# Kernel optimization log

Measured on AMD Instinct MI355X. Metric: run time of the kernel, lower is better.

The kernel has to match this reference:

```python
import jax, jax.numpy as jnp
import numpy as np

TEMPERATURE = 0.07
EPS = 1e-07


def setup_inputs() -> dict:
    key = jax.random.key(0)
    kf, kl = jax.random.split(key)
    bsz, n_views, d = 4096, 2, 256
    feats = jax.random.normal(kf, (bsz, n_views, d), dtype=jnp.float32)
    # L2-normalize per view, as in standard SupCon pipelines
    feats = feats / jnp.linalg.norm(feats, axis=-1, keepdims=True)
    labels = jax.random.randint(kl, (bsz,), 0, 3, dtype=jnp.int64 if jax.config.jax_enable_x64 else jnp.int32)
    return {"features": feats, "labels": labels}


def reference(features, labels):
    bsz, n_views, d = features.shape
    n = bsz * n_views
    # torch.cat(torch.unbind(features, dim=1), dim=0): views stacked along batch
    contrast_feature = jnp.transpose(features, (1, 0, 2)).reshape(n, d)
    anchor_feature = contrast_feature  # contrast_mode == 'all'

    # label-equality mask with the module's 1e-7 offset, tiled over views
    mask_small = (labels[:, None] == labels[None, :]).astype(jnp.float32) + EPS
    mask = jnp.tile(mask_small, (n_views, n_views))  # [n, n]

    logits_mask = 1.0 - jnp.eye(n, dtype=jnp.float32)  # zero out self-contrast
    mask_pos = mask * logits_mask
    mask_neg = (1.0 - mask) * logits_mask

    similarity = jnp.exp(jnp.matmul(anchor_feature, contrast_feature.T) / TEMPERATURE)
    pos = jnp.sum(similarity * mask_pos, axis=1)
    neg = jnp.sum(similarity * mask_neg, axis=1)
    loss = -jnp.mean(jnp.log(pos / (pos + neg)))
    return loss
```

## Files before the change

### kernel.cpp

```cpp
#include <hip/hip_runtime.h>
#include <cstdint>

#define BSZ   4096
#define NTOT  8192
#define DIM   256
#define BT    128
#define BKE   64
#define NCB   (NTOT / BT)
#define INV_T (1.0f/0.07f)

typedef __bf16 bf16x8 __attribute__((ext_vector_type(8)));
typedef float  f32x4  __attribute__((ext_vector_type(4)));

#define GLOAD_LDS16(gp, lp)                                                  \
  __builtin_amdgcn_global_load_lds(                                          \
      (const __attribute__((address_space(1))) void*)(gp),                   \
      (__attribute__((address_space(3))) void*)(lp), 16, 0, 0)

__device__ __forceinline__ unsigned short f2bf(float f) {
  unsigned int u = __float_as_uint(f);
  u = u + 0x7FFFu + ((u >> 16) & 1u);
  return (unsigned short)(u >> 16);
}

__global__ __launch_bounds__(256) void cvt_kernel(const float* __restrict__ F,
                                                  unsigned short* __restrict__ X,
                                                  float* __restrict__ gsum,
                                                  int* __restrict__ gcnt) {
  if (blockIdx.x == 0 && threadIdx.x == 0) { *gsum = 0.f; *gcnt = 0; }
  int t = blockIdx.x * 256 + threadIdx.x;
  int r = t >> 6;
  int k = (t & 63) << 2;
  const float4 v = *(const float4*)(F + (size_t)(r & (BSZ - 1)) * (2 * DIM)
                                      + (r >> 12) * DIM + k);
  ushort4 o = make_ushort4(f2bf(v.x), f2bf(v.y), f2bf(v.z), f2bf(v.w));
  *(ushort4*)(X + (size_t)r * DIM + k) = o;
}

__global__ __launch_bounds__(256) void supcon_kernel(
    const unsigned short* __restrict__ X, const int* __restrict__ lab,
    float* __restrict__ partTot, float* __restrict__ partEq) {
  __shared__ unsigned short lA[BT * BKE];
  __shared__ unsigned short lB[BT * BKE];

  const int tid  = threadIdx.x;
  const int lane = tid & 63;
  const int wave = tid >> 6;
  const int wr   = (wave >> 1) * 64;
  const int wc   = (wave & 1) * 64;
  const int l15  = lane & 15;
  const int quad = lane >> 4;

  const int b = blockIdx.x;
  int j = (int)((sqrtf(8.f * (float)b + 1.f) - 1.f) * 0.5f);
  while ((j + 1) * (j + 2) / 2 <= b) ++j;
  while (j * (j + 1) / 2 > b) --j;
  const int i  = b - j * (j + 1) / 2;
  const int RB = i * BT;
  const int CB = j * BT;

  const int srow8  = lane >> 3;
  const int schunk = (lane & 7) ^ srow8;
  const unsigned short* gA = X + (size_t)(RB + wave * 32 + srow8) * DIM + schunk * 8;
  const unsigned short* gB = X + (size_t)(CB + wave * 32 + srow8) * DIM + schunk * 8;

  f32x4 acc[4][4] = {};

  for (int kb = 0; kb < DIM; kb += BKE) {
    __syncthreads();
#pragma unroll
    for (int l = 0; l < 4; ++l) {
      GLOAD_LDS16(gA + (size_t)l * 8 * DIM + kb, lA + (wave * 32 + l * 8) * BKE);
      GLOAD_LDS16(gB + (size_t)l * 8 * DIM + kb, lB + (wave * 32 + l * 8) * BKE);
    }
    __syncthreads();

#pragma unroll
    for (int sub = 0; sub < 2; ++sub) {
      bf16x8 aF[4], bF[4];
      const int slot = ((sub * 4 + quad) ^ (l15 & 7)) * 8;
#pragma unroll
      for (int t = 0; t < 4; ++t) {
        aF[t] = *(const bf16x8*)(lA + (wr + t * 16 + l15) * BKE + slot);
        bF[t] = *(const bf16x8*)(lB + (wc + t * 16 + l15) * BKE + slot);
      }
#pragma unroll
      for (int tr = 0; tr < 4; ++tr)
#pragma unroll
        for (int tc = 0; tc < 4; ++tc)
          acc[tr][tc] = __builtin_amdgcn_mfma_f32_16x16x32_bf16(
              aF[tr], bF[tc], acc[tr][tc], 0, 0, 0);
    }
  }

  int colIdx[4], colLab[4];
#pragma unroll
  for (int tc = 0; tc < 4; ++tc) {
    colIdx[tc] = CB + wc + tc * 16 + l15;
    colLab[tc] = lab[colIdx[tc] & (BSZ - 1)];
  }
  int rowLab[4][4];
#pragma unroll
  for (int tr = 0; tr < 4; ++tr)
#pragma unroll
    for (int reg = 0; reg < 4; ++reg)
      rowLab[tr][reg] = lab[(RB + wr + tr * 16 + quad * 4 + reg) & (BSZ - 1)];

  if (i == j) {
#pragma unroll
    for (int tr = 0; tr < 4; ++tr)
#pragma unroll
      for (int tc = 0; tc < 4; ++tc)
#pragma unroll
        for (int reg = 0; reg < 4; ++reg) {
          const int row = RB + wr + tr * 16 + quad * 4 + reg;
          float e = __expf(acc[tr][tc][reg] * INV_T);
          acc[tr][tc][reg] = (colIdx[tc] == row) ? 0.f : e;
        }
  } else {
#pragma unroll
    for (int tr = 0; tr < 4; ++tr)
#pragma unroll
      for (int tc = 0; tc < 4; ++tc)
#pragma unroll
        for (int reg = 0; reg < 4; ++reg)
          acc[tr][tc][reg] = __expf(acc[tr][tc][reg] * INV_T);
  }

  __syncthreads();
  float* sbuf = (float*)lA;
#pragma unroll
  for (int tr = 0; tr < 4; ++tr) {
#pragma unroll
    for (int reg = 0; reg < 4; ++reg) {
      float tot = 0.f, eqs = 0.f;
#pragma unroll
      for (int tc = 0; tc < 4; ++tc) {
        const float e = acc[tr][tc][reg];
        tot += e;
        if (colLab[tc] == rowLab[tr][reg]) eqs += e;
      }
#pragma unroll
      for (int off = 1; off < 16; off <<= 1) {
        tot += __shfl_xor(tot, off, 64);
        eqs += __shfl_xor(eqs, off, 64);
      }
      if (l15 == 0) {
        const int rl_ = wr + tr * 16 + quad * 4 + reg;
        sbuf[(wave & 1) * 128 + rl_]       = tot;
        sbuf[256 + (wave & 1) * 128 + rl_] = eqs;
      }
    }
  }
  if (i != j) {
#pragma unroll
    for (int tc = 0; tc < 4; ++tc) {
      float tt = 0.f, te = 0.f;
#pragma unroll
      for (int tr = 0; tr < 4; ++tr)
#pragma unroll
        for (int reg = 0; reg < 4; ++reg) {
          const float e = acc[tr][tc][reg];
          tt += e;
          if (rowLab[tr][reg] == colLab[tc]) te += e;
        }
      tt += __shfl_xor(tt, 16, 64);  te += __shfl_xor(te, 16, 64);
      tt += __shfl_xor(tt, 32, 64);  te += __shfl_xor(te, 32, 64);
      if (quad == 0) {
        const int cl_ = wc + tc * 16 + l15;
        sbuf[512 + (wave >> 1) * 128 + cl_] = tt;
        sbuf[768 + (wave >> 1) * 128 + cl_] = te;
      }
    }
  }
  __syncthreads();

  if (tid < 128) {
    partTot[(size_t)j * NTOT + RB + tid] = sbuf[tid] + sbuf[128 + tid];
    partEq [(size_t)j * NTOT + RB + tid] = sbuf[256 + tid] + sbuf[384 + tid];
  } else if (i != j) {
    const int c = tid - 128;
    partTot[(size_t)i * NTOT + CB + c] = sbuf[512 + c] + sbuf[640 + c];
    partEq [(size_t)i * NTOT + CB + c] = sbuf[768 + c] + sbuf[896 + c];
  }
}

__global__ __launch_bounds__(256) void reduce_kernel(
    const float* __restrict__ partTot, const float* __restrict__ partEq,
    float* __restrict__ gsum, int* __restrict__ gcnt,
    unsigned int* __restrict__ out) {
  const int r = blockIdx.x * 256 + threadIdx.x;
  float tot = 0.f, eqs = 0.f;
#pragma unroll 8
  for (int cb = 0; cb < NCB; ++cb) {
    tot += partTot[(size_t)cb * NTOT + r];
    eqs += partEq [(size_t)cb * NTOT + r];
  }
  const float term = __logf((eqs + 1e-7f * tot) / tot);
  __shared__ float red[256];
  red[threadIdx.x] = term;
  __syncthreads();
  for (int step = 128; step > 0; step >>= 1) {
    if (threadIdx.x < step) red[threadIdx.x] += red[threadIdx.x + step];
    __syncthreads();
  }
  if (threadIdx.x == 0) {
    atomicAdd(gsum, red[0]);
    __threadfence();
    const int old = atomicAdd(gcnt, 1);
    if (old == (int)gridDim.x - 1) {
      __threadfence();
      const float total = atomicAdd(gsum, 0.0f);
      const float loss = -total / (float)NTOT;
      const unsigned short bb = f2bf(loss);
      out[0] = ((unsigned int)bb << 16) | (unsigned int)bb;
    }
  }
}

extern "C" void kernel_launch(void* const* d_in, const int* in_sizes, int n_in,
                              void* d_out, int out_size, void* d_ws, size_t ws_size,
                              hipStream_t stream) {
  (void)in_sizes; (void)n_in; (void)out_size; (void)ws_size;
  const float* feats = (const float*)d_in[0];
  const int*   labels = (const int*)d_in[1];

  char* ws = (char*)d_ws;
  unsigned short* X = (unsigned short*)ws;
  float* partTot = (float*)(ws + (size_t)NTOT * DIM * 2);
  float* partEq  = partTot + (size_t)NCB * NTOT;
  float* gsum    = partEq  + (size_t)NCB * NTOT;
  int*   gcnt    = (int*)(gsum + 1);

  cvt_kernel<<<NTOT * DIM / 4 / 256, 256, 0, stream>>>(feats, X, gsum, gcnt);
  supcon_kernel<<<NCB * (NCB + 1) / 2, 256, 0, stream>>>(X, labels, partTot, partEq);
  reduce_kernel<<<NTOT / 256, 256, 0, stream>>>(partTot, partEq, gsum, gcnt,
                                                (unsigned int*)d_out);
}
```

Before: 116.5 us.

## Group triangular tiles by XCD with swizzled mapping and widen K-step to 128

Block indices are remapped so that consecutive blocks on each XCD (b&7) cover an 8x8 group of tiles, which should improve L2 reuse of the row and column panels. The K-tile doubles from 64 to 128, halving the number of load/sync iterations, and the LDS XOR swizzle is widened to 16 chunks to match. Label loads are hoisted ahead of the GEMM loop so their latency can hide behind it. The reduce kernel now uses 128-thread blocks, giving twice as many blocks. Costs: LDS per block doubles to 64KB, which may reduce occupancy, and the hardcoded tile mapping constants only hold for this problem size.

```diff
diff --git a/kernel.cpp b/kernel.cpp
--- a/kernel.cpp
+++ b/kernel.cpp
@@ -5,8 +5,9 @@
 #define NTOT  8192
 #define DIM   256
 #define BT    128
-#define BKE   64
+#define BKE   128
 #define NCB   (NTOT / BT)
+#define NBLK  (NCB * (NCB + 1) / 2)
 #define INV_T (1.0f/0.07f)
 
 typedef __bf16 bf16x8 __attribute__((ext_vector_type(8)));
@@ -52,33 +53,63 @@
   const int quad = lane >> 4;
 
   const int b = blockIdx.x;
-  int j = (int)((sqrtf(8.f * (float)b + 1.f) - 1.f) * 0.5f);
-  while ((j + 1) * (j + 2) / 2 <= b) ++j;
-  while (j * (j + 1) / 2 > b) --j;
-  const int i  = b - j * (j + 1) / 2;
+  const int c = (b & 7) * (NBLK / 8) + (b >> 3);
+  int i, j;
+  if (c < 1792) {
+    const int spo = c >> 6;
+    const int w   = c & 63;
+    int g1 = 0, rem = spo;
+    while (rem >= 7 - g1) { rem -= 7 - g1; ++g1; }
+    const int g2 = g1 + 1 + rem;
+    i = g1 * 8 + (w >> 3);
+    j = g2 * 8 + (w & 7);
+  } else {
+    const int c2 = c - 1792;
+    const int g  = c2 / 36;
+    int w = c2 - g * 36;
+    int a = 0;
+    while (w >= 8 - a) { w -= 8 - a; ++a; }
+    i = g * 8 + a;
+    j = g * 8 + a + w;
+  }
   const int RB = i * BT;
   const int CB = j * BT;
 
-  const int srow8  = lane >> 3;
-  const int schunk = (lane & 7) ^ srow8;
-  const unsigned short* gA = X + (size_t)(RB + wave * 32 + srow8) * DIM + schunk * 8;
-  const unsigned short* gB = X + (size_t)(CB + wave * 32 + srow8) * DIM + schunk * 8;
+  int colIdx[4], colLab[4];
+#pragma unroll
+  for (int tc = 0; tc < 4; ++tc) {
+    colIdx[tc] = CB + wc + tc * 16 + l15;
+    colLab[tc] = lab[colIdx[tc] & (BSZ - 1)];
+  }
+  int rowLab[4][4];
+#pragma unroll
+  for (int tr = 0; tr < 4; ++tr)
+#pragma unroll
+    for (int reg = 0; reg < 4; ++reg)
+      rowLab[tr][reg] = lab[(RB + wr + tr * 16 + quad * 4 + reg) & (BSZ - 1)];
+
+  const int srow  = lane >> 4;
+  const unsigned short* gA = X + (size_t)(RB + wave * 32 + srow) * DIM;
+  const unsigned short* gB = X + (size_t)(CB + wave * 32 + srow) * DIM;
 
   f32x4 acc[4][4] = {};
 
   for (int kb = 0; kb < DIM; kb += BKE) {
     __syncthreads();
 #pragma unroll
-    for (int l = 0; l < 4; ++l) {
-      GLOAD_LDS16(gA + (size_t)l * 8 * DIM + kb, lA + (wave * 32 + l * 8) * BKE);
-      GLOAD_LDS16(gB + (size_t)l * 8 * DIM + kb, lB + (wave * 32 + l * 8) * BKE);
+    for (int l = 0; l < 8; ++l) {
+      const int chunk = (lane & 15) ^ ((l * 4 + srow) & 15);
+      GLOAD_LDS16(gA + (size_t)(l * 4) * DIM + kb + chunk * 8,
+                  lA + (wave * 32 + l * 4) * BKE);
+      GLOAD_LDS16(gB + (size_t)(l * 4) * DIM + kb + chunk * 8,
+                  lB + (wave * 32 + l * 4) * BKE);
     }
     __syncthreads();
 
 #pragma unroll
-    for (int sub = 0; sub < 2; ++sub) {
+    for (int sub = 0; sub < 4; ++sub) {
       bf16x8 aF[4], bF[4];
-      const int slot = ((sub * 4 + quad) ^ (l15 & 7)) * 8;
+      const int slot = ((sub * 4 + quad) ^ l15) * 8;
 #pragma unroll
       for (int t = 0; t < 4; ++t) {
         aF[t] = *(const bf16x8*)(lA + (wr + t * 16 + l15) * BKE + slot);
@@ -92,19 +123,6 @@
               aF[tr], bF[tc], acc[tr][tc], 0, 0, 0);
     }
   }
-
-  int colIdx[4], colLab[4];
-#pragma unroll
-  for (int tc = 0; tc < 4; ++tc) {
-    colIdx[tc] = CB + wc + tc * 16 + l15;
-    colLab[tc] = lab[colIdx[tc] & (BSZ - 1)];
-  }
-  int rowLab[4][4];
-#pragma unroll
-  for (int tr = 0; tr < 4; ++tr)
-#pragma unroll
-    for (int reg = 0; reg < 4; ++reg)
-      rowLab[tr][reg] = lab[(RB + wr + tr * 16 + quad * 4 + reg) & (BSZ - 1)];
 
   if (i == j) {
 #pragma unroll
@@ -179,17 +197,17 @@
     partTot[(size_t)j * NTOT + RB + tid] = sbuf[tid] + sbuf[128 + tid];
     partEq [(size_t)j * NTOT + RB + tid] = sbuf[256 + tid] + sbuf[384 + tid];
   } else if (i != j) {
-    const int c = tid - 128;
-    partTot[(size_t)i * NTOT + CB + c] = sbuf[512 + c] + sbuf[640 + c];
-    partEq [(size_t)i * NTOT + CB + c] = sbuf[768 + c] + sbuf[896 + c];
-  }
-}
-
-__global__ __launch_bounds__(256) void reduce_kernel(
+    const int c2 = tid - 128;
+    partTot[(size_t)i * NTOT + CB + c2] = sbuf[512 + c2] + sbuf[640 + c2];
+    partEq [(size_t)i * NTOT + CB + c2] = sbuf[768 + c2] + sbuf[896 + c2];
+  }
+}
+
+__global__ __launch_bounds__(128) void reduce_kernel(
     const float* __restrict__ partTot, const float* __restrict__ partEq,
     float* __restrict__ gsum, int* __restrict__ gcnt,
     unsigned int* __restrict__ out) {
-  const int r = blockIdx.x * 256 + threadIdx.x;
+  const int r = blockIdx.x * 128 + threadIdx.x;
   float tot = 0.f, eqs = 0.f;
 #pragma unroll 8
   for (int cb = 0; cb < NCB; ++cb) {
@@ -197,10 +215,10 @@
     eqs += partEq [(size_t)cb * NTOT + r];
   }
   const float term = __logf((eqs + 1e-7f * tot) / tot);
-  __shared__ float red[256];
+  __shared__ float red[128];
   red[threadIdx.x] = term;
   __syncthreads();
-  for (int step = 128; step > 0; step >>= 1) {
+  for (int step = 64; step > 0; step >>= 1) {
     if (threadIdx.x < step) red[threadIdx.x] += red[threadIdx.x + step];
     __syncthreads();
   }
@@ -233,7 +251,7 @@
   int*   gcnt    = (int*)(gsum + 1);
 
   cvt_kernel<<<NTOT * DIM / 4 / 256, 256, 0, stream>>>(feats, X, gsum, gcnt);
-  supcon_kernel<<<NCB * (NCB + 1) / 2, 256, 0, stream>>>(X, labels, partTot, partEq);
-  reduce_kernel<<<NTOT / 256, 256, 0, stream>>>(partTot, partEq, gsum, gcnt,
+  supcon_kernel<<<NBLK, 256, 0, stream>>>(X, labels, partTot, partEq);
+  reduce_kernel<<<NTOT / 128, 128, 0, stream>>>(partTot, partEq, gsum, gcnt,
                                                 (unsigned int*)d_out);
 }
```

Result: no change. 115.0 us (-1.3%).
